# Optimization experiments

Measured on AMD Instinct MI355X. Metric: run time of the kernel, lower is better.

## Reference

```python
import jax, jax.numpy as jnp
import numpy as np


def setup_inputs() -> dict:
    key = jax.random.key(0)
    k1, k2, k3 = jax.random.split(key, 3)
    early = jax.random.normal(k1, (64, 1, 512, 512), dtype=jnp.float32)
    middle = jax.random.normal(k2, (64, 1, 256, 256), dtype=jnp.float32)
    deep = jax.random.normal(k3, (64, 1, 128, 128), dtype=jnp.float32)
    return {"early": early, "middle": middle, "deep": deep, "max_features": 500000}


def reference(early, middle, deep, max_features):
    # Concatenate all scores and find the threshold = (max_features)-th entry of
    # the descending sort, i.e. the (max_features+1)-th largest value.
    all_scores = jnp.concatenate([early.ravel(), middle.ravel(), deep.ravel()])
    n = all_scores.shape[0]
    if max_features >= n:
        thresh = jnp.asarray(0.0, dtype=all_scores.dtype)
    else:
        # top_k(k+1)[-1] == sort(descending)[k]; avoids a full sort.
        topk_vals, _ = jax.lax.top_k(all_scores, max_features + 1)
        thresh = topk_vals[-1]
    thresh = jax.lax.stop_gradient(thresh)
    early_out = jnp.where(early < thresh, jnp.zeros((), early.dtype), early)
    middle_out = jnp.where(middle < thresh, jnp.zeros((), middle.dtype), middle)
    deep_out = jnp.where(deep < thresh, jnp.zeros((), deep.dtype), deep)
    return (early_out, middle_out, deep_out)
```

## Files before the change

kernel.cpp:

```cpp
#include <hip/hip_runtime.h>

typedef float nfloat4 __attribute__((ext_vector_type(4)));

#define WS_CANDCNT 0
#define WS_B1      1
#define WS_K2      2
#define WS_PFX     3
#define WS_K3      4
#define WS_HIST1   16
#define WS_HIST2   272
#define WS_HIST3   4368
#define WS_ZEND    8464
#define WS_CAND    8464

#define STASH 2048

__device__ __forceinline__ unsigned fkey(float f) {
  unsigned x = __float_as_uint(f);
  return x ^ ((x & 0x80000000u) ? 0xFFFFFFFFu : 0x80000000u);
}
__device__ __forceinline__ float unkey(unsigned u) {
  unsigned x = u ^ ((u & 0x80000000u) ? 0x80000000u : 0xFFFFFFFFu);
  return __uint_as_float(x);
}

__device__ __forceinline__ unsigned block_scan_incl(unsigned v, unsigned* sh4) {
  const int t = threadIdx.x;
  unsigned p = v;
#pragma unroll
  for (int off = 1; off < 64; off <<= 1) {
    unsigned y = __shfl_up(p, off);
    if ((t & 63) >= off) p += y;
  }
  if ((t & 63) == 63) sh4[t >> 6] = p;
  __syncthreads();
  unsigned wo = 0;
  for (int w = 0; w < (t >> 6); ++w) wo += sh4[w];
  __syncthreads();
  return p + wo;
}

__device__ __forceinline__ uint2 select_desc256(const unsigned* __restrict__ gh,
                                                unsigned k, unsigned* sh4, unsigned* sel2) {
  const int t = threadIdx.x;
  unsigned cnt = gh[255 - t];
  unsigned incl = block_scan_incl(cnt, sh4);
  unsigned excl = incl - cnt;
  if (excl < k && incl >= k) { sel2[0] = (unsigned)(255 - t); sel2[1] = k - excl; }
  __syncthreads();
  uint2 r; r.x = sel2[0]; r.y = sel2[1];
  __syncthreads();
  return r;
}

__device__ __forceinline__ uint2 select_desc4096(const unsigned* __restrict__ gh,
                                                 unsigned k, unsigned* sh4, unsigned* sel2) {
  const int t = threadIdx.x;
  unsigned loc[16]; unsigned s = 0;
  const int base = 4095 - t * 16;
#pragma unroll
  for (int j = 0; j < 16; ++j) { unsigned c = gh[base - j]; loc[j] = c; s += c; }
  unsigned incl = block_scan_incl(s, sh4);
  unsigned excl = incl - s;
  if (excl < k && incl >= k) {
    unsigned cum = excl; int j = 0;
    while (cum + loc[j] < k) { cum += loc[j]; ++j; }
    sel2[0] = (unsigned)(base - j); sel2[1] = k - cum;
  }
  __syncthreads();
  uint2 r; r.x = sel2[0]; r.y = sel2[1];
  __syncthreads();
  return r;
}

__global__ void zero_ws(unsigned* __restrict__ ws) {
  int i = blockIdx.x * blockDim.x + threadIdx.x;
  if (i < WS_ZEND) ws[i] = 0u;
}

__global__ void __launch_bounds__(1024) hist1_kernel(
    const float* __restrict__ e, const float* __restrict__ m,
    const float* __restrict__ d, int n0v, int n1v, int n2v,
    unsigned* __restrict__ ws) {
  __shared__ unsigned h[256 * 32];
  for (int i = threadIdx.x; i < 256 * 32; i += 1024) h[i] = 0u;
  __syncthreads();
  const unsigned sub = threadIdx.x & 31u;
  const int gid = blockIdx.x * 1024 + threadIdx.x;
  const int G = gridDim.x * 1024;

  auto acc1 = [&](float4 f) {
    atomicAdd(&h[((fkey(f.x) >> 24) << 5) | sub], 1u);
    atomicAdd(&h[((fkey(f.y) >> 24) << 5) | sub], 1u);
    atomicAdd(&h[((fkey(f.z) >> 24) << 5) | sub], 1u);
    atomicAdd(&h[((fkey(f.w) >> 24) << 5) | sub], 1u);
  };
  auto sweep = [&](const float* src, int nv) {
    const float4* a4 = (const float4*)src;
    int v = gid;
    for (; v + 3 * G < nv; v += 4 * G) {
      float4 f0 = a4[v];
      float4 f1 = a4[v + G];
      float4 f2 = a4[v + 2 * G];
      float4 f3 = a4[v + 3 * G];
      acc1(f0); acc1(f1); acc1(f2); acc1(f3);
    }
    for (; v < nv; v += G) acc1(a4[v]);
  };
  sweep(e, n0v);
  sweep(m, n1v);
  sweep(d, n2v);
  __syncthreads();
  const int t = threadIdx.x;
  if (t < 256) {
    unsigned s = 0;
#pragma unroll
    for (int j = 0; j < 32; ++j) s += h[(t << 5) + ((t + j) & 31)];
    if (s) atomicAdd(&ws[WS_HIST1 + t], s);
  }
}

__global__ void __launch_bounds__(256) sel1_kernel(
    const int* __restrict__ maxf, unsigned* __restrict__ ws, long long n) {
  __shared__ unsigned sh4[4];
  __shared__ unsigned sel2[2];
  long long kk = (long long)maxf[0] + 1;
  if (kk > n) {
    if (threadIdx.x == 0) ws[WS_B1] = 0x80u;
    return;
  }
  uint2 r = select_desc256(ws + WS_HIST1, (unsigned)kk, sh4, sel2);
  if (threadIdx.x == 0) { ws[WS_B1] = r.x; ws[WS_K2] = r.y; }
}

__global__ void __launch_bounds__(1024) scatter_kernel(
    const float* __restrict__ e, const float* __restrict__ m, const float* __restrict__ d,
    float* __restrict__ out, unsigned* __restrict__ ws, unsigned cap,
    int e_blks, int m_blks) {
  const int t = threadIdx.x;
  const int bid = blockIdx.x;

  __shared__ float    sh_v[STASH];
  __shared__ unsigned sh_i[STASH];
  __shared__ unsigned sh_cnt;
  __shared__ unsigned sh_base;

  if (t == 0) sh_cnt = 0u;
  const unsigned b1 = ws[WS_B1];
  __syncthreads();

  const float4* in4;
  if (bid < e_blks)               in4 = (const float4*)e + (long long)bid * 2048;
  else if (bid < e_blks + m_blks) in4 = (const float4*)m + (long long)(bid - e_blks) * 2048;
  else                            in4 = (const float4*)d + (long long)(bid - e_blks - m_blks) * 2048;
  const int out_base_v = bid * 2048;
  nfloat4* out4 = (nfloat4*)out + out_base_v;

  float* gcV = (float*)(ws + WS_CAND);
  unsigned* gcI = ws + WS_CAND + cap;

  auto emit1 = [&](float4 f, int v) {
    unsigned kx = fkey(f.x), ky = fkey(f.y), kz = fkey(f.z), kw = fkey(f.w);
    nfloat4 o;
    o.x = ((kx >> 24) >= b1) ? f.x : 0.0f;
    o.y = ((ky >> 24) >= b1) ? f.y : 0.0f;
    o.z = ((kz >> 24) >= b1) ? f.z : 0.0f;
    o.w = ((kw >> 24) >= b1) ? f.w : 0.0f;
    __builtin_nontemporal_store(o, &out4[v]);
    unsigned ks[4] = {kx, ky, kz, kw};
    float fs[4] = {f.x, f.y, f.z, f.w};
#pragma unroll
    for (int cc = 0; cc < 4; ++cc) {
      if ((ks[cc] >> 24) == b1) {
        unsigned idx = (unsigned)(out_base_v + v) * 4u + (unsigned)cc;
        unsigned pos = atomicAdd(&sh_cnt, 1u);
        if (pos < STASH) { sh_v[pos] = fs[cc]; sh_i[pos] = idx; }
        else {
          unsigned g = atomicAdd(&ws[WS_CANDCNT], 1u);
          gcV[g] = fs[cc]; gcI[g] = idx;
        }
      }
    }
  };

  const int v0 = t;
  const int v1 = 1024 + t;
  float4 f0 = in4[v0];
  float4 f1 = in4[v1];
  emit1(f0, v0);
  emit1(f1, v1);

  __syncthreads();
  if (t == 0) {
    unsigned tot = sh_cnt < STASH ? sh_cnt : STASH;
    sh_base = tot ? atomicAdd(&ws[WS_CANDCNT], tot) : 0u;
    sh_cnt = tot;
  }
  __syncthreads();
  const unsigned tot = sh_cnt;
  const unsigned base = sh_base;
  for (unsigned i = t; i < tot; i += 1024) {
    gcV[base + i] = sh_v[i];
    gcI[base + i] = sh_i[i];
  }
}

__global__ void __launch_bounds__(256) candhist2_kernel(
    unsigned* __restrict__ ws, unsigned cap) {
  const int t = threadIdx.x;
  __shared__ unsigned sh_hist[4096];
  for (int i = t; i < 4096; i += 256) sh_hist[i] = 0u;
  __syncthreads();
  unsigned cnt = ws[WS_CANDCNT]; if (cnt > cap) cnt = cap;
  const float* candV = (const float*)(ws + WS_CAND);
  const unsigned G = gridDim.x * 256;
  for (unsigned i = blockIdx.x * 256 + t; i < cnt; i += G) {
    unsigned u = fkey(candV[i]);
    atomicAdd(&sh_hist[(u >> 12) & 0xFFFu], 1u);
  }
  __syncthreads();
  for (int i = t; i < 4096; i += 256) {
    unsigned v = sh_hist[i];
    if (v) atomicAdd(&ws[WS_HIST2 + i], v);
  }
}

__global__ void __launch_bounds__(256) candhist3_kernel(
    const int* __restrict__ maxf, unsigned* __restrict__ ws, unsigned cap, long long n) {
  const int t = threadIdx.x;
  __shared__ unsigned sh_hist[4096];
  __shared__ unsigned sh4[4];
  __shared__ unsigned sel2[2];
  for (int i = t; i < 4096; i += 256) sh_hist[i] = 0u;

  long long kk = (long long)maxf[0] + 1;
  unsigned pfx;
  if (kk > n) {
    pfx = 0x80u << 12;
    __syncthreads();
  } else {
    unsigned b1 = ws[WS_B1];
    unsigned k2 = ws[WS_K2];
    uint2 r2 = select_desc4096(ws + WS_HIST2, k2, sh4, sel2);
    pfx = (b1 << 12) | r2.x;
    if (blockIdx.x == 0 && t == 0) { ws[WS_PFX] = pfx; ws[WS_K3] = r2.y; }
  }
  __syncthreads();

  unsigned cnt = ws[WS_CANDCNT]; if (cnt > cap) cnt = cap;
  const float* candV = (const float*)(ws + WS_CAND);
  const unsigned G = gridDim.x * 256;
  for (unsigned i = blockIdx.x * 256 + t; i < cnt; i += G) {
    unsigned u = fkey(candV[i]);
    if ((u >> 12) == pfx) atomicAdd(&sh_hist[u & 0xFFFu], 1u);
  }
  __syncthreads();
  for (int i = t; i < 4096; i += 256) {
    unsigned v = sh_hist[i];
    if (v) atomicAdd(&ws[WS_HIST3 + i], v);
  }
}

__global__ void __launch_bounds__(256) fixup_kernel(
    float* __restrict__ out, const int* __restrict__ maxf,
    unsigned* __restrict__ ws, unsigned cap, long long n) {
  const int t = threadIdx.x;
  __shared__ unsigned sh4[4];
  __shared__ unsigned sel2[2];

  long long kk = (long long)maxf[0] + 1;
  float th;
  if (kk > n) {
    th = 0.0f;
    __syncthreads();
  } else {
    unsigned pfx = ws[WS_PFX];
    unsigned k3  = ws[WS_K3];
    uint2 r3 = select_desc4096(ws + WS_HIST3, k3, sh4, sel2);
    th = unkey((pfx << 12) | r3.x);
  }

  unsigned cnt = ws[WS_CANDCNT]; if (cnt > cap) cnt = cap;
  const float* candV = (const float*)(ws + WS_CAND);
  const unsigned* candI = ws + WS_CAND + cap;
  const unsigned G = gridDim.x * 256;
  for (unsigned i = blockIdx.x * 256 + t; i < cnt; i += G) {
    float f = candV[i];
    if (f < th) out[candI[i]] = 0.0f;
  }
}

extern "C" void kernel_launch(void* const* d_in, const int* in_sizes, int n_in,
                              void* d_out, int out_size, void* d_ws, size_t ws_size,
                              hipStream_t stream) {
  const float* e = (const float*)d_in[0];
  const float* m = (const float*)d_in[1];
  const float* d = (const float*)d_in[2];
  const int* maxf = (const int*)d_in[3];
  float* out = (float*)d_out;
  unsigned* ws = (unsigned*)d_ws;

  const long long n0 = in_sizes[0], n1 = in_sizes[1], n2 = in_sizes[2];
  const long long n = n0 + n1 + n2;
  const int n0v = (int)(n0 / 4), n1v = (int)(n1 / 4), n2v = (int)(n2 / 4);

  long long capll = ((long long)(ws_size / 4) - WS_CAND) / 2;
  if (capll < 0) capll = 0;
  if (capll > n) capll = n;
  const unsigned cap = (unsigned)capll;

  const int e_blks = (int)(n0 / 8192), m_blks = (int)(n1 / 8192);
  const int nblocks = (int)(n / 8192);

  zero_ws<<<(WS_ZEND + 255) / 256, 256, 0, stream>>>(ws);
  hist1_kernel<<<512, 1024, 0, stream>>>(e, m, d, n0v, n1v, n2v, ws);
  sel1_kernel<<<1, 256, 0, stream>>>(maxf, ws, n);
  scatter_kernel<<<nblocks, 1024, 0, stream>>>(e, m, d, out, ws, cap, e_blks, m_blks);
  candhist2_kernel<<<128, 256, 0, stream>>>(ws, cap);
  candhist3_kernel<<<128, 256, 0, stream>>>(maxf, ws, cap, n);
  fixup_kernel<<<256, 256, 0, stream>>>(out, maxf, ws, cap, n);
}
```

Before: 210.2 us.

## Fuse radix-select pipeline into one cooperative persistent kernel with grid syncs

Replaces the seven-kernel sequence (zero, histogram, select, scatter, two candidate histograms, fixup) with a single cooperative kernel that separates the stages with grid.sync, and falls back to the old launches if the cooperative launch fails. Each block redundantly computes the bucket selection from the global histograms, which removes the separate single-block select kernels. Kernel launch gaps and inter-kernel drain are the target. In exchange the scatter pass now runs as a persistent grid-stride loop over tiles with a per-block stash that is flushed only at the end, which can overflow to global atomics more often. Grid barriers and reduced occupancy (at most 512 blocks) add their own cost.

```diff
diff --git a/kernel.cpp b/kernel.cpp
--- a/kernel.cpp
+++ b/kernel.cpp
@@ -1,4 +1,7 @@
 #include <hip/hip_runtime.h>
+#include <hip/hip_cooperative_groups.h>
+
+namespace cg = cooperative_groups;
 
 typedef float nfloat4 __attribute__((ext_vector_type(4)));
 
@@ -14,6 +17,7 @@
 #define WS_CAND    8464
 
 #define STASH 2048
+#define NTHR  1024
 
 __device__ __forceinline__ unsigned fkey(float f) {
   unsigned x = __float_as_uint(f);
@@ -22,6 +26,240 @@
 __device__ __forceinline__ float unkey(unsigned u) {
   unsigned x = u ^ ((u & 0x80000000u) ? 0x80000000u : 0xFFFFFFFFu);
   return __uint_as_float(x);
+}
+
+__device__ __forceinline__ unsigned scan1024(unsigned v, unsigned* sh16) {
+  const int t = threadIdx.x;
+  unsigned p = v;
+#pragma unroll
+  for (int off = 1; off < 64; off <<= 1) {
+    unsigned y = __shfl_up(p, off);
+    if ((t & 63) >= off) p += y;
+  }
+  if ((t & 63) == 63) sh16[t >> 6] = p;
+  __syncthreads();
+  unsigned wo = 0;
+  for (int w = 0; w < (t >> 6); ++w) wo += sh16[w];
+  __syncthreads();
+  return p + wo;
+}
+
+__device__ __forceinline__ uint2 sel256_w(const unsigned* __restrict__ gh, unsigned k,
+                                          unsigned* sh16, unsigned* sel2) {
+  const int t = threadIdx.x;
+  unsigned cnt = (t < 256) ? gh[255 - t] : 0u;
+  unsigned incl = scan1024(cnt, sh16);
+  unsigned excl = incl - cnt;
+  if (t < 256 && excl < k && incl >= k) { sel2[0] = (unsigned)(255 - t); sel2[1] = k - excl; }
+  __syncthreads();
+  uint2 r; r.x = sel2[0]; r.y = sel2[1];
+  __syncthreads();
+  return r;
+}
+
+__device__ __forceinline__ uint2 sel4096_w(const unsigned* __restrict__ gh, unsigned k,
+                                           unsigned* sh16, unsigned* sel2) {
+  const int t = threadIdx.x;
+  unsigned loc[4]; unsigned s = 0;
+  const int base = 4095 - t * 4;
+#pragma unroll
+  for (int j = 0; j < 4; ++j) { unsigned c = gh[base - j]; loc[j] = c; s += c; }
+  unsigned incl = scan1024(s, sh16);
+  unsigned excl = incl - s;
+  if (excl < k && incl >= k) {
+    unsigned cum = excl; int j = 0;
+    while (cum + loc[j] < k) { cum += loc[j]; ++j; }
+    sel2[0] = (unsigned)(base - j); sel2[1] = k - cum;
+  }
+  __syncthreads();
+  uint2 r; r.x = sel2[0]; r.y = sel2[1];
+  __syncthreads();
+  return r;
+}
+
+__global__ void __launch_bounds__(NTHR, 8) mega_kernel(
+    const float* __restrict__ e, const float* __restrict__ m, const float* __restrict__ d,
+    const int* __restrict__ maxf, float* __restrict__ out, unsigned* __restrict__ ws,
+    unsigned cap, int n0v, int n1v, int n2v,
+    int e_blks, int m_blks, int nblocks, long long n) {
+  cg::grid_group grid = cg::this_grid();
+  const int t = threadIdx.x;
+  const int bid = blockIdx.x;
+  const int NB = gridDim.x;
+
+  __shared__ unsigned shraw[256 * 32];
+  __shared__ unsigned sh16[16];
+  __shared__ unsigned sel2[2];
+  __shared__ unsigned sh_cnt, sh_base;
+
+  for (int i = bid * NTHR + t; i < WS_ZEND; i += NB * NTHR) ws[i] = 0u;
+  __threadfence();
+  grid.sync();
+
+  {
+    unsigned* h = shraw;
+    for (int i = t; i < 256 * 32; i += NTHR) h[i] = 0u;
+    __syncthreads();
+    const unsigned sub = t & 31u;
+    const int gid = bid * NTHR + t;
+    const int G = NB * NTHR;
+    auto acc1 = [&](float4 f) {
+      atomicAdd(&h[((fkey(f.x) >> 24) << 5) | sub], 1u);
+      atomicAdd(&h[((fkey(f.y) >> 24) << 5) | sub], 1u);
+      atomicAdd(&h[((fkey(f.z) >> 24) << 5) | sub], 1u);
+      atomicAdd(&h[((fkey(f.w) >> 24) << 5) | sub], 1u);
+    };
+    auto sweep = [&](const float* src, int nv) {
+      const float4* a4 = (const float4*)src;
+      int v = gid;
+      for (; v + 3 * G < nv; v += 4 * G) {
+        float4 f0 = a4[v];
+        float4 f1 = a4[v + G];
+        float4 f2 = a4[v + 2 * G];
+        float4 f3 = a4[v + 3 * G];
+        acc1(f0); acc1(f1); acc1(f2); acc1(f3);
+      }
+      for (; v < nv; v += G) acc1(a4[v]);
+    };
+    sweep(e, n0v);
+    sweep(m, n1v);
+    sweep(d, n2v);
+    __syncthreads();
+    if (t < 256) {
+      unsigned s = 0;
+#pragma unroll
+      for (int j = 0; j < 32; ++j) s += h[(t << 5) + ((t + j) & 31)];
+      if (s) atomicAdd(&ws[WS_HIST1 + t], s);
+    }
+  }
+  __threadfence();
+  grid.sync();
+
+  const long long kk = (long long)maxf[0] + 1;
+  const bool bigk = (kk > n);
+  unsigned b1, k2 = 0;
+  if (bigk) {
+    b1 = 0x80u;
+  } else {
+    uint2 r1 = sel256_w(ws + WS_HIST1, (unsigned)kk, sh16, sel2);
+    b1 = r1.x; k2 = r1.y;
+  }
+
+  {
+    float*    sh_v = (float*)shraw;
+    unsigned* sh_i = shraw + STASH;
+    if (t == 0) sh_cnt = 0u;
+    __syncthreads();
+    float* gcV = (float*)(ws + WS_CAND);
+    unsigned* gcI = ws + WS_CAND + cap;
+
+    for (int tile = bid; tile < nblocks; tile += NB) {
+      const float4* in4;
+      if (tile < e_blks)               in4 = (const float4*)e + (long long)tile * 2048;
+      else if (tile < e_blks + m_blks) in4 = (const float4*)m + (long long)(tile - e_blks) * 2048;
+      else                             in4 = (const float4*)d + (long long)(tile - e_blks - m_blks) * 2048;
+      const int out_base_v = tile * 2048;
+      nfloat4* out4 = (nfloat4*)out + out_base_v;
+
+      auto emit1 = [&](float4 f, int v) {
+        unsigned kx = fkey(f.x), ky = fkey(f.y), kz = fkey(f.z), kw = fkey(f.w);
+        nfloat4 o;
+        o.x = ((kx >> 24) >= b1) ? f.x : 0.0f;
+        o.y = ((ky >> 24) >= b1) ? f.y : 0.0f;
+        o.z = ((kz >> 24) >= b1) ? f.z : 0.0f;
+        o.w = ((kw >> 24) >= b1) ? f.w : 0.0f;
+        __builtin_nontemporal_store(o, &out4[v]);
+        unsigned ks[4] = {kx, ky, kz, kw};
+        float fs[4] = {f.x, f.y, f.z, f.w};
+#pragma unroll
+        for (int cc = 0; cc < 4; ++cc) {
+          if ((ks[cc] >> 24) == b1) {
+            unsigned idx = (unsigned)(out_base_v + v) * 4u + (unsigned)cc;
+            unsigned pos = atomicAdd(&sh_cnt, 1u);
+            if (pos < STASH) { sh_v[pos] = fs[cc]; sh_i[pos] = idx; }
+            else {
+              unsigned g = atomicAdd(&ws[WS_CANDCNT], 1u);
+              gcV[g] = fs[cc]; gcI[g] = idx;
+            }
+          }
+        }
+      };
+      float4 f0 = in4[t];
+      float4 f1 = in4[1024 + t];
+      emit1(f0, t);
+      emit1(f1, 1024 + t);
+    }
+
+    __syncthreads();
+    if (t == 0) {
+      unsigned tot = sh_cnt < STASH ? sh_cnt : STASH;
+      sh_base = tot ? atomicAdd(&ws[WS_CANDCNT], tot) : 0u;
+      sh_cnt = tot;
+    }
+    __syncthreads();
+    const unsigned tot = sh_cnt;
+    const unsigned base = sh_base;
+    for (unsigned i = t; i < tot; i += NTHR) {
+      gcV[base + i] = sh_v[i];
+      gcI[base + i] = sh_i[i];
+    }
+  }
+  __threadfence();
+  grid.sync();
+
+  const unsigned cnt0 = ws[WS_CANDCNT];
+  const unsigned cnt = cnt0 > cap ? cap : cnt0;
+  const float* candV = (const float*)(ws + WS_CAND);
+  const unsigned* candI = ws + WS_CAND + cap;
+  const int chb = NB < 128 ? NB : 128;
+
+  if (!bigk) {
+    if (bid < chb) {
+      unsigned* sh_hist = shraw;
+      for (int i = t; i < 4096; i += NTHR) sh_hist[i] = 0u;
+      __syncthreads();
+      for (unsigned i = (unsigned)bid * NTHR + t; i < cnt; i += (unsigned)chb * NTHR)
+        atomicAdd(&sh_hist[(fkey(candV[i]) >> 12) & 0xFFFu], 1u);
+      __syncthreads();
+      for (int i = t; i < 4096; i += NTHR) {
+        unsigned v = sh_hist[i];
+        if (v) atomicAdd(&ws[WS_HIST2 + i], v);
+      }
+    }
+  }
+  __threadfence();
+  grid.sync();
+
+  unsigned pfx = 0, k3 = 0;
+  if (!bigk) {
+    uint2 r2 = sel4096_w(ws + WS_HIST2, k2, sh16, sel2);
+    pfx = (b1 << 12) | r2.x; k3 = r2.y;
+    if (bid < chb) {
+      unsigned* sh_hist = shraw;
+      for (int i = t; i < 4096; i += NTHR) sh_hist[i] = 0u;
+      __syncthreads();
+      for (unsigned i = (unsigned)bid * NTHR + t; i < cnt; i += (unsigned)chb * NTHR) {
+        unsigned u = fkey(candV[i]);
+        if ((u >> 12) == pfx) atomicAdd(&sh_hist[u & 0xFFFu], 1u);
+      }
+      __syncthreads();
+      for (int i = t; i < 4096; i += NTHR) {
+        unsigned v = sh_hist[i];
+        if (v) atomicAdd(&ws[WS_HIST3 + i], v);
+      }
+    }
+  }
+  __threadfence();
+  grid.sync();
+
+  if (!bigk) {
+    uint2 r3 = sel4096_w(ws + WS_HIST3, k3, sh16, sel2);
+    const float th = unkey((pfx << 12) | r3.x);
+    for (unsigned i = (unsigned)bid * NTHR + t; i < cnt; i += (unsigned)NB * NTHR) {
+      float f = candV[i];
+      if (f < th) out[candI[i]] = 0.0f;
+    }
+  }
 }
 
 __device__ __forceinline__ unsigned block_scan_incl(unsigned v, unsigned* sh4) {
@@ -88,7 +326,6 @@
   const unsigned sub = threadIdx.x & 31u;
   const int gid = blockIdx.x * 1024 + threadIdx.x;
   const int G = gridDim.x * 1024;
-
   auto acc1 = [&](float4 f) {
     atomicAdd(&h[((fkey(f.x) >> 24) << 5) | sub], 1u);
     atomicAdd(&h[((fkey(f.y) >> 24) << 5) | sub], 1u);
@@ -99,17 +336,13 @@
     const float4* a4 = (const float4*)src;
     int v = gid;
     for (; v + 3 * G < nv; v += 4 * G) {
-      float4 f0 = a4[v];
-      float4 f1 = a4[v + G];
-      float4 f2 = a4[v + 2 * G];
-      float4 f3 = a4[v + 3 * G];
+      float4 f0 = a4[v]; float4 f1 = a4[v + G];
+      float4 f2 = a4[v + 2 * G]; float4 f3 = a4[v + 3 * G];
       acc1(f0); acc1(f1); acc1(f2); acc1(f3);
     }
     for (; v < nv; v += G) acc1(a4[v]);
   };
-  sweep(e, n0v);
-  sweep(m, n1v);
-  sweep(d, n2v);
+  sweep(e, n0v); sweep(m, n1v); sweep(d, n2v);
   __syncthreads();
   const int t = threadIdx.x;
   if (t < 256) {
@@ -139,26 +372,21 @@
     int e_blks, int m_blks) {
   const int t = threadIdx.x;
   const int bid = blockIdx.x;
-
   __shared__ float    sh_v[STASH];
   __shared__ unsigned sh_i[STASH];
   __shared__ unsigned sh_cnt;
   __shared__ unsigned sh_base;
-
   if (t == 0) sh_cnt = 0u;
   const unsigned b1 = ws[WS_B1];
   __syncthreads();
-
   const float4* in4;
   if (bid < e_blks)               in4 = (const float4*)e + (long long)bid * 2048;
   else if (bid < e_blks + m_blks) in4 = (const float4*)m + (long long)(bid - e_blks) * 2048;
   else                            in4 = (const float4*)d + (long long)(bid - e_blks - m_blks) * 2048;
   const int out_base_v = bid * 2048;
   nfloat4* out4 = (nfloat4*)out + out_base_v;
-
   float* gcV = (float*)(ws + WS_CAND);
   unsigned* gcI = ws + WS_CAND + cap;
-
   auto emit1 = [&](float4 f, int v) {
     unsigned kx = fkey(f.x), ky = fkey(f.y), kz = fkey(f.z), kw = fkey(f.w);
     nfloat4 o;
@@ -182,14 +410,10 @@
       }
     }
   };
-
-  const int v0 = t;
-  const int v1 = 1024 + t;
-  float4 f0 = in4[v0];
-  float4 f1 = in4[v1];
-  emit1(f0, v0);
-  emit1(f1, v1);
-
+  float4 f0 = in4[t];
+  float4 f1 = in4[1024 + t];
+  emit1(f0, t);
+  emit1(f1, 1024 + t);
   __syncthreads();
   if (t == 0) {
     unsigned tot = sh_cnt < STASH ? sh_cnt : STASH;
@@ -232,7 +456,6 @@
   __shared__ unsigned sh4[4];
   __shared__ unsigned sel2[2];
   for (int i = t; i < 4096; i += 256) sh_hist[i] = 0u;
-
   long long kk = (long long)maxf[0] + 1;
   unsigned pfx;
   if (kk > n) {
@@ -246,7 +469,6 @@
     if (blockIdx.x == 0 && t == 0) { ws[WS_PFX] = pfx; ws[WS_K3] = r2.y; }
   }
   __syncthreads();
-
   unsigned cnt = ws[WS_CANDCNT]; if (cnt > cap) cnt = cap;
   const float* candV = (const float*)(ws + WS_CAND);
   const unsigned G = gridDim.x * 256;
@@ -267,7 +489,6 @@
   const int t = threadIdx.x;
   __shared__ unsigned sh4[4];
   __shared__ unsigned sel2[2];
-
   long long kk = (long long)maxf[0] + 1;
   float th;
   if (kk > n) {
@@ -279,7 +500,6 @@
     uint2 r3 = select_desc4096(ws + WS_HIST3, k3, sh4, sel2);
     th = unkey((pfx << 12) | r3.x);
   }
-
   unsigned cnt = ws[WS_CANDCNT]; if (cnt > cap) cnt = cap;
   const float* candV = (const float*)(ws + WS_CAND);
   const unsigned* candI = ws + WS_CAND + cap;
@@ -312,11 +532,24 @@
   const int e_blks = (int)(n0 / 8192), m_blks = (int)(n1 / 8192);
   const int nblocks = (int)(n / 8192);
 
-  zero_ws<<<(WS_ZEND + 255) / 256, 256, 0, stream>>>(ws);
-  hist1_kernel<<<512, 1024, 0, stream>>>(e, m, d, n0v, n1v, n2v, ws);
-  sel1_kernel<<<1, 256, 0, stream>>>(maxf, ws, n);
-  scatter_kernel<<<nblocks, 1024, 0, stream>>>(e, m, d, out, ws, cap, e_blks, m_blks);
-  candhist2_kernel<<<128, 256, 0, stream>>>(ws, cap);
-  candhist3_kernel<<<128, 256, 0, stream>>>(maxf, ws, cap, n);
-  fixup_kernel<<<256, 256, 0, stream>>>(out, maxf, ws, cap, n);
-}
+  int maxb = 0;
+  if (hipOccupancyMaxActiveBlocksPerMultiprocessor(&maxb, mega_kernel, NTHR, 0) != hipSuccess ||
+      maxb < 1) maxb = 1;
+  int nb = maxb * 256;
+  if (nb > 512) nb = 512;
+
+  void* args[] = {(void*)&e, (void*)&m, (void*)&d, (void*)&maxf, (void*)&out, (void*)&ws,
+                  (void*)&cap, (void*)&n0v, (void*)&n1v, (void*)&n2v,
+                  (void*)&e_blks, (void*)&m_blks, (void*)&nblocks, (void*)&n};
+  hipError_t err = hipLaunchCooperativeKernel(mega_kernel, dim3(nb), dim3(NTHR),
+                                              args, 0, stream);
+  if (err != hipSuccess) {
+    zero_ws<<<(WS_ZEND + 255) / 256, 256, 0, stream>>>(ws);
+    hist1_kernel<<<512, 1024, 0, stream>>>(e, m, d, n0v, n1v, n2v, ws);
+    sel1_kernel<<<1, 256, 0, stream>>>(maxf, ws, n);
+    scatter_kernel<<<nblocks, 1024, 0, stream>>>(e, m, d, out, ws, cap, e_blks, m_blks);
+    candhist2_kernel<<<128, 256, 0, stream>>>(ws, cap);
+    candhist3_kernel<<<128, 256, 0, stream>>>(maxf, ws, cap, n);
+    fixup_kernel<<<256, 256, 0, stream>>>(out, maxf, ws, cap, n);
+  }
+}
```

Measured after the change: 679.2 us. +223.1%, slower.

## Fold selection steps into last-block epilogues and drop separate kernels

Applied to the files above, without the earlier changes.

Removes the standalone sel1 kernel by having the last hist1 block, detected with a done-counter atomic and threadfence, perform the first-digit selection. The second and third digit selections move into last-block epilogues of candhist2 and candhist3, so later kernels just read a precomputed prefix or threshold instead of every block redoing the 4096-bin scan. The zero kernel becomes a hipMemsetAsync. The aim is fewer launches and less redundant per-block scan work, at the cost of extra atomics and fences at each block's end.

```diff
diff --git a/kernel.cpp b/kernel.cpp
--- a/kernel.cpp
+++ b/kernel.cpp
@@ -7,6 +7,10 @@
 #define WS_K2      2
 #define WS_PFX     3
 #define WS_K3      4
+#define WS_TH      5
+#define WS_DONE1   8
+#define WS_DONE2   9
+#define WS_DONE3   10
 #define WS_HIST1   16
 #define WS_HIST2   272
 #define WS_HIST3   4368
@@ -38,19 +42,6 @@
   for (int w = 0; w < (t >> 6); ++w) wo += sh4[w];
   __syncthreads();
   return p + wo;
-}
-
-__device__ __forceinline__ uint2 select_desc256(const unsigned* __restrict__ gh,
-                                                unsigned k, unsigned* sh4, unsigned* sel2) {
-  const int t = threadIdx.x;
-  unsigned cnt = gh[255 - t];
-  unsigned incl = block_scan_incl(cnt, sh4);
-  unsigned excl = incl - cnt;
-  if (excl < k && incl >= k) { sel2[0] = (unsigned)(255 - t); sel2[1] = k - excl; }
-  __syncthreads();
-  uint2 r; r.x = sel2[0]; r.y = sel2[1];
-  __syncthreads();
-  return r;
 }
 
 __device__ __forceinline__ uint2 select_desc4096(const unsigned* __restrict__ gh,
@@ -73,16 +64,43 @@
   return r;
 }
 
-__global__ void zero_ws(unsigned* __restrict__ ws) {
-  int i = blockIdx.x * blockDim.x + threadIdx.x;
-  if (i < WS_ZEND) ws[i] = 0u;
+__device__ __forceinline__ unsigned scan1024(unsigned v, unsigned* sh16) {
+  const int t = threadIdx.x;
+  unsigned p = v;
+#pragma unroll
+  for (int off = 1; off < 64; off <<= 1) {
+    unsigned y = __shfl_up(p, off);
+    if ((t & 63) >= off) p += y;
+  }
+  if ((t & 63) == 63) sh16[t >> 6] = p;
+  __syncthreads();
+  unsigned wo = 0;
+  for (int w = 0; w < (t >> 6); ++w) wo += sh16[w];
+  __syncthreads();
+  return p + wo;
+}
+
+__device__ __forceinline__ uint2 sel256_w(const unsigned* __restrict__ gh, unsigned k,
+                                          unsigned* sh16, unsigned* sel2) {
+  const int t = threadIdx.x;
+  unsigned cnt = (t < 256) ? gh[255 - t] : 0u;
+  unsigned incl = scan1024(cnt, sh16);
+  unsigned excl = incl - cnt;
+  if (t < 256 && excl < k && incl >= k) { sel2[0] = (unsigned)(255 - t); sel2[1] = k - excl; }
+  __syncthreads();
+  uint2 r; r.x = sel2[0]; r.y = sel2[1];
+  __syncthreads();
+  return r;
 }
 
 __global__ void __launch_bounds__(1024) hist1_kernel(
     const float* __restrict__ e, const float* __restrict__ m,
     const float* __restrict__ d, int n0v, int n1v, int n2v,
-    unsigned* __restrict__ ws) {
+    unsigned* __restrict__ ws, const int* __restrict__ maxf, long long n) {
   __shared__ unsigned h[256 * 32];
+  __shared__ unsigned sh16[16];
+  __shared__ unsigned sel2[2];
+  __shared__ unsigned sh_last;
   for (int i = threadIdx.x; i < 256 * 32; i += 1024) h[i] = 0u;
   __syncthreads();
   const unsigned sub = threadIdx.x & 31u;
@@ -99,17 +117,13 @@
     const float4* a4 = (const float4*)src;
     int v = gid;
     for (; v + 3 * G < nv; v += 4 * G) {
-      float4 f0 = a4[v];
-      float4 f1 = a4[v + G];
-      float4 f2 = a4[v + 2 * G];
-      float4 f3 = a4[v + 3 * G];
+      float4 f0 = a4[v]; float4 f1 = a4[v + G];
+      float4 f2 = a4[v + 2 * G]; float4 f3 = a4[v + 3 * G];
       acc1(f0); acc1(f1); acc1(f2); acc1(f3);
     }
     for (; v < nv; v += G) acc1(a4[v]);
   };
-  sweep(e, n0v);
-  sweep(m, n1v);
-  sweep(d, n2v);
+  sweep(e, n0v); sweep(m, n1v); sweep(d, n2v);
   __syncthreads();
   const int t = threadIdx.x;
   if (t < 256) {
@@ -118,19 +132,23 @@
     for (int j = 0; j < 32; ++j) s += h[(t << 5) + ((t + j) & 31)];
     if (s) atomicAdd(&ws[WS_HIST1 + t], s);
   }
-}
-
-__global__ void __launch_bounds__(256) sel1_kernel(
-    const int* __restrict__ maxf, unsigned* __restrict__ ws, long long n) {
-  __shared__ unsigned sh4[4];
-  __shared__ unsigned sel2[2];
-  long long kk = (long long)maxf[0] + 1;
-  if (kk > n) {
-    if (threadIdx.x == 0) ws[WS_B1] = 0x80u;
-    return;
-  }
-  uint2 r = select_desc256(ws + WS_HIST1, (unsigned)kk, sh4, sel2);
-  if (threadIdx.x == 0) { ws[WS_B1] = r.x; ws[WS_K2] = r.y; }
+  __syncthreads();
+  if (t == 0) {
+    __threadfence();
+    unsigned old = atomicAdd(&ws[WS_DONE1], 1u);
+    sh_last = (old == gridDim.x - 1u) ? 1u : 0u;
+  }
+  __syncthreads();
+  if (sh_last) {
+    __threadfence();
+    long long kk = (long long)maxf[0] + 1;
+    if (kk > n) {
+      if (t == 0) ws[WS_B1] = 0x80u;
+    } else {
+      uint2 r = sel256_w(ws + WS_HIST1, (unsigned)kk, sh16, sel2);
+      if (t == 0) { ws[WS_B1] = r.x; ws[WS_K2] = r.y; }
+    }
+  }
 }
 
 __global__ void __launch_bounds__(1024) scatter_kernel(
@@ -139,26 +157,21 @@
     int e_blks, int m_blks) {
   const int t = threadIdx.x;
   const int bid = blockIdx.x;
-
   __shared__ float    sh_v[STASH];
   __shared__ unsigned sh_i[STASH];
   __shared__ unsigned sh_cnt;
   __shared__ unsigned sh_base;
-
   if (t == 0) sh_cnt = 0u;
   const unsigned b1 = ws[WS_B1];
   __syncthreads();
-
   const float4* in4;
   if (bid < e_blks)               in4 = (const float4*)e + (long long)bid * 2048;
   else if (bid < e_blks + m_blks) in4 = (const float4*)m + (long long)(bid - e_blks) * 2048;
   else                            in4 = (const float4*)d + (long long)(bid - e_blks - m_blks) * 2048;
   const int out_base_v = bid * 2048;
   nfloat4* out4 = (nfloat4*)out + out_base_v;
-
   float* gcV = (float*)(ws + WS_CAND);
   unsigned* gcI = ws + WS_CAND + cap;
-
   auto emit1 = [&](float4 f, int v) {
     unsigned kx = fkey(f.x), ky = fkey(f.y), kz = fkey(f.z), kw = fkey(f.w);
     nfloat4 o;
@@ -182,14 +195,10 @@
       }
     }
   };
-
-  const int v0 = t;
-  const int v1 = 1024 + t;
-  float4 f0 = in4[v0];
-  float4 f1 = in4[v1];
-  emit1(f0, v0);
-  emit1(f1, v1);
-
+  float4 f0 = in4[t];
+  float4 f1 = in4[1024 + t];
+  emit1(f0, t);
+  emit1(f1, 1024 + t);
   __syncthreads();
   if (t == 0) {
     unsigned tot = sh_cnt < STASH ? sh_cnt : STASH;
@@ -206,9 +215,12 @@
 }
 
 __global__ void __launch_bounds__(256) candhist2_kernel(
-    unsigned* __restrict__ ws, unsigned cap) {
+    const int* __restrict__ maxf, unsigned* __restrict__ ws, unsigned cap, long long n) {
   const int t = threadIdx.x;
   __shared__ unsigned sh_hist[4096];
+  __shared__ unsigned sh4[4];
+  __shared__ unsigned sel2[2];
+  __shared__ unsigned sh_last;
   for (int i = t; i < 4096; i += 256) sh_hist[i] = 0u;
   __syncthreads();
   unsigned cnt = ws[WS_CANDCNT]; if (cnt > cap) cnt = cap;
@@ -223,6 +235,23 @@
     unsigned v = sh_hist[i];
     if (v) atomicAdd(&ws[WS_HIST2 + i], v);
   }
+  __syncthreads();
+  if (t == 0) {
+    __threadfence();
+    unsigned old = atomicAdd(&ws[WS_DONE2], 1u);
+    sh_last = (old == gridDim.x - 1u) ? 1u : 0u;
+  }
+  __syncthreads();
+  if (sh_last) {
+    __threadfence();
+    long long kk = (long long)maxf[0] + 1;
+    if (kk <= n) {
+      unsigned b1 = ws[WS_B1];
+      unsigned k2 = ws[WS_K2];
+      uint2 r2 = select_desc4096(ws + WS_HIST2, k2, sh4, sel2);
+      if (t == 0) { ws[WS_PFX] = (b1 << 12) | r2.x; ws[WS_K3] = r2.y; }
+    }
+  }
 }
 
 __global__ void __launch_bounds__(256) candhist3_kernel(
@@ -231,22 +260,10 @@
   __shared__ unsigned sh_hist[4096];
   __shared__ unsigned sh4[4];
   __shared__ unsigned sel2[2];
+  __shared__ unsigned sh_last;
   for (int i = t; i < 4096; i += 256) sh_hist[i] = 0u;
-
-  long long kk = (long long)maxf[0] + 1;
-  unsigned pfx;
-  if (kk > n) {
-    pfx = 0x80u << 12;
-    __syncthreads();
-  } else {
-    unsigned b1 = ws[WS_B1];
-    unsigned k2 = ws[WS_K2];
-    uint2 r2 = select_desc4096(ws + WS_HIST2, k2, sh4, sel2);
-    pfx = (b1 << 12) | r2.x;
-    if (blockIdx.x == 0 && t == 0) { ws[WS_PFX] = pfx; ws[WS_K3] = r2.y; }
-  }
-  __syncthreads();
-
+  __syncthreads();
+  const unsigned pfx = ws[WS_PFX];
   unsigned cnt = ws[WS_CANDCNT]; if (cnt > cap) cnt = cap;
   const float* candV = (const float*)(ws + WS_CAND);
   const unsigned G = gridDim.x * 256;
@@ -259,27 +276,30 @@
     unsigned v = sh_hist[i];
     if (v) atomicAdd(&ws[WS_HIST3 + i], v);
   }
+  __syncthreads();
+  if (t == 0) {
+    __threadfence();
+    unsigned old = atomicAdd(&ws[WS_DONE3], 1u);
+    sh_last = (old == gridDim.x - 1u) ? 1u : 0u;
+  }
+  __syncthreads();
+  if (sh_last) {
+    __threadfence();
+    long long kk = (long long)maxf[0] + 1;
+    if (kk > n) {
+      if (t == 0) ws[WS_TH] = __float_as_uint(0.0f);
+    } else {
+      unsigned k3 = ws[WS_K3];
+      uint2 r3 = select_desc4096(ws + WS_HIST3, k3, sh4, sel2);
+      if (t == 0) ws[WS_TH] = __float_as_uint(unkey((pfx << 12) | r3.x));
+    }
+  }
 }
 
 __global__ void __launch_bounds__(256) fixup_kernel(
-    float* __restrict__ out, const int* __restrict__ maxf,
-    unsigned* __restrict__ ws, unsigned cap, long long n) {
-  const int t = threadIdx.x;
-  __shared__ unsigned sh4[4];
-  __shared__ unsigned sel2[2];
-
-  long long kk = (long long)maxf[0] + 1;
-  float th;
-  if (kk > n) {
-    th = 0.0f;
-    __syncthreads();
-  } else {
-    unsigned pfx = ws[WS_PFX];
-    unsigned k3  = ws[WS_K3];
-    uint2 r3 = select_desc4096(ws + WS_HIST3, k3, sh4, sel2);
-    th = unkey((pfx << 12) | r3.x);
-  }
-
+    float* __restrict__ out, unsigned* __restrict__ ws, unsigned cap) {
+  const int t = threadIdx.x;
+  const float th = __uint_as_float(ws[WS_TH]);
   unsigned cnt = ws[WS_CANDCNT]; if (cnt > cap) cnt = cap;
   const float* candV = (const float*)(ws + WS_CAND);
   const unsigned* candI = ws + WS_CAND + cap;
@@ -312,11 +332,10 @@
   const int e_blks = (int)(n0 / 8192), m_blks = (int)(n1 / 8192);
   const int nblocks = (int)(n / 8192);
 
-  zero_ws<<<(WS_ZEND + 255) / 256, 256, 0, stream>>>(ws);
-  hist1_kernel<<<512, 1024, 0, stream>>>(e, m, d, n0v, n1v, n2v, ws);
-  sel1_kernel<<<1, 256, 0, stream>>>(maxf, ws, n);
+  hipMemsetAsync(ws, 0, WS_ZEND * sizeof(unsigned), stream);
+  hist1_kernel<<<512, 1024, 0, stream>>>(e, m, d, n0v, n1v, n2v, ws, maxf, n);
   scatter_kernel<<<nblocks, 1024, 0, stream>>>(e, m, d, out, ws, cap, e_blks, m_blks);
-  candhist2_kernel<<<128, 256, 0, stream>>>(ws, cap);
+  candhist2_kernel<<<128, 256, 0, stream>>>(maxf, ws, cap, n);
   candhist3_kernel<<<128, 256, 0, stream>>>(maxf, ws, cap, n);
-  fixup_kernel<<<256, 256, 0, stream>>>(out, maxf, ws, cap, n);
-}
+  fixup_kernel<<<256, 256, 0, stream>>>(out, ws, cap);
+}
```

Result: slower. 225.5 us (+7.3%).
